# Kernel optimization log

Hardware: AMD Instinct MI355X
Metric: run time of the kernel (lower is better)

## Reference

```python
import jax, jax.numpy as jnp
import numpy as np
import math

B, L, D = 4, 512, 768
H, DH, R = 12, 64, 128


def _layernorm(x, g, b, eps=1e-5):
    mu = jnp.mean(x, axis=-1, keepdims=True)
    var = jnp.var(x, axis=-1, keepdims=True)
    return (x - mu) * jax.lax.rsqrt(var + eps) * g + b


def setup_inputs() -> dict:
    key = jax.random.key(0)
    ks = jax.random.split(key, 8)
    s = 0.02
    return {
        "x": jax.random.normal(ks[0], (B, L, D), jnp.float32),
        "W_qkv": jax.random.normal(ks[1], (D, 3 * D), jnp.float32) * s,
        "b_qkv": jnp.zeros((3 * D,), jnp.float32),
        "W_b1": jax.random.normal(ks[2], (D, R), jnp.float32) * s,
        "W_b2": jax.random.normal(ks[3], (R, H * 5), jnp.float32) * s,
        "temperature": jnp.ones((1,), jnp.float32) * 0.5,
        "W_proj": jax.random.normal(ks[4], (D, D), jnp.float32) * s,
        "b_proj": jnp.zeros((D,), jnp.float32),
        "ln_g": jnp.ones((D,), jnp.float32),
        "ln_b": jnp.zeros((D,), jnp.float32),
        "mem_g": jnp.ones((DH,), jnp.float32),
        "mem_b": jnp.zeros((DH,), jnp.float32),
    }


def reference(x, W_qkv, b_qkv, W_b1, W_b2, temperature, W_proj, b_proj, ln_g, ln_b, mem_g, mem_b):
    Bq, Lq, Dq = x.shape
    xn = _layernorm(x, ln_g, ln_b)
    qkv = xn @ W_qkv + b_qkv
    q, k, v = jnp.split(qkv, 3, axis=-1)

    # bottleneck gating params: (B, L, H, 5)
    params = (jax.nn.silu(x @ W_b1) @ W_b2).reshape(Bq, Lq, H, 5)
    sem_amp = jax.nn.sigmoid(params[..., 0])
    sem_phase = jnp.tanh(params[..., 1]) * math.pi
    ctx_amp = jax.nn.sigmoid(params[..., 2])
    ctx_phase = jnp.tanh(params[..., 3]) * math.pi
    decay = 0.5 + 0.49 * jax.nn.sigmoid(params[..., 4])  # (B,L,H)

    temp = jnp.clip(temperature, 0.1, 2.0)  # (1,) broadcasts
    interference = jnp.tanh(sem_amp * ctx_amp * jnp.cos(sem_phase - ctx_phase)) * temp
    gate = jax.nn.sigmoid(interference)  # (B,L,H)

    qf = (jax.nn.elu(q) + 1.0).reshape(Bq, Lq, H, DH)
    kf = (jax.nn.elu(k) + 1.0).reshape(Bq, Lq, H, DH)
    vf = v.reshape(Bq, Lq, H, DH)

    log_decay = jnp.log(decay + 1e-8)
    cld = jnp.maximum(jnp.cumsum(log_decay, axis=1), -85.0)  # (B,L,H)
    df = jnp.exp(cld)
    inv_df = jnp.exp(-cld)
    ema = 1.0 - decay  # (B,L,H)

    # kv outer products gated by interference: (B,L,H,DH,DH)
    kv_all = jnp.einsum('blhd,blhe->blhde', kf, vf) * (1.0 + gate)[..., None, None]
    kv_states = jnp.cumsum(kv_all * (ema * inv_df)[..., None, None], axis=1) * df[..., None, None]

    z_states = jnp.cumsum(kf * (ema * inv_df)[..., None], axis=1) * df[..., None]  # (B,L,H,DH)

    out_num = jnp.einsum('blhd,blhde->blhe', qf, kv_states)
    den = jnp.sum(qf * z_states, axis=-1, keepdims=True) + 1e-6
    out = out_num / den  # (B,L,H,DH)

    out = _layernorm(out, mem_g, mem_b)
    attn_out = out.reshape(Bq, Lq, Dq)
    return attn_out @ W_proj + b_proj, gate
```

## Files before the change

### kernel.cpp

```cpp
#include <hip/hip_runtime.h>
#include <math.h>

#define PI_F 3.14159265358979323846f

static constexpr int L_ = 512, D_ = 768, H_ = 12, DH_ = 64;
static constexpr int BL_ = 2048;
static constexpr int BLD_ = BL_ * D_;
static constexpr int NC_ = 8;
static constexpr int BH_ = 48;

__global__ void sentinel_kernel(float* out, float code, float aux) {
  out[0] = code; out[1] = aux;
}

__global__ __launch_bounds__(256) void ln_stats(const float* __restrict__ x,
                                                float* __restrict__ murs) {
  int row = blockIdx.x, tid = threadIdx.x;
  const float* xr = x + (size_t)row * D_;
  float v0 = xr[tid], v1 = xr[tid + 256], v2 = xr[tid + 512];
  float s = v0 + v1 + v2;
  float s2 = v0 * v0 + v1 * v1 + v2 * v2;
#pragma unroll
  for (int off = 32; off > 0; off >>= 1) { s += __shfl_xor(s, off); s2 += __shfl_xor(s2, off); }
  __shared__ float red[8];
  if ((tid & 63) == 0) { red[tid >> 6] = s; red[4 + (tid >> 6)] = s2; }
  __syncthreads();
  if (tid == 0) {
    float st = red[0] + red[1] + red[2] + red[3];
    float qt = red[4] + red[5] + red[6] + red[7];
    float mu = st * (1.0f / D_);
    float var = qt * (1.0f / D_) - mu * mu;
    murs[2 * row] = mu;
    murs[2 * row + 1] = rsqrtf(var + 1e-5f);
  }
}

__global__ __launch_bounds__(128) void gemm_qkv(const float* __restrict__ x,
                                                const float* __restrict__ murs,
                                                const float* __restrict__ lg,
                                                const float* __restrict__ lb,
                                                const float* __restrict__ Bm,
                                                const float* __restrict__ bias,
                                                float* __restrict__ Oq,
                                                float* __restrict__ Ok,
                                                float* __restrict__ Ov) {
  const int N = 2304, K = 768;
  __shared__ float As[16][68];
  __shared__ float Bs[16][68];
  int tid = threadIdx.x;
  int tx = tid & 15, ty = tid >> 4;
  int row0 = blockIdx.y * 64, col0 = blockIdx.x * 64;
  float acc[8][4] = {};
  int ar = tid >> 1, ak = (tid & 1) * 8;
  int bk = tid >> 3, bc = (tid & 7) * 8;
  float2 m2 = *(const float2*)&murs[2 * (row0 + ar)];
  float mu = m2.x, rs = m2.y;
  const float* Arow = x + (size_t)(row0 + ar) * K;
  for (int k0 = 0; k0 < K; k0 += 16) {
    float4 a0 = *(const float4*)&Arow[k0 + ak];
    float4 a1 = *(const float4*)&Arow[k0 + ak + 4];
    float4 g0 = *(const float4*)&lg[k0 + ak];
    float4 g1 = *(const float4*)&lg[k0 + ak + 4];
    float4 c0 = *(const float4*)&lb[k0 + ak];
    float4 c1 = *(const float4*)&lb[k0 + ak + 4];
    a0.x = (a0.x - mu) * rs * g0.x + c0.x;
    a0.y = (a0.y - mu) * rs * g0.y + c0.y;
    a0.z = (a0.z - mu) * rs * g0.z + c0.z;
    a0.w = (a0.w - mu) * rs * g0.w + c0.w;
    a1.x = (a1.x - mu) * rs * g1.x + c1.x;
    a1.y = (a1.y - mu) * rs * g1.y + c1.y;
    a1.z = (a1.z - mu) * rs * g1.z + c1.z;
    a1.w = (a1.w - mu) * rs * g1.w + c1.w;
    As[ak + 0][ar] = a0.x; As[ak + 1][ar] = a0.y;
    As[ak + 2][ar] = a0.z; As[ak + 3][ar] = a0.w;
    As[ak + 4][ar] = a1.x; As[ak + 5][ar] = a1.y;
    As[ak + 6][ar] = a1.z; As[ak + 7][ar] = a1.w;
    *(float4*)&Bs[bk][bc]     = *(const float4*)&Bm[(size_t)(k0 + bk) * N + col0 + bc];
    *(float4*)&Bs[bk][bc + 4] = *(const float4*)&Bm[(size_t)(k0 + bk) * N + col0 + bc + 4];
    __syncthreads();
#pragma unroll
    for (int kk = 0; kk < 16; ++kk) {
      float4 av0 = *(float4*)&As[kk][ty * 8];
      float4 av1 = *(float4*)&As[kk][ty * 8 + 4];
      float4 bv = *(float4*)&Bs[kk][tx * 4];
      acc[0][0] += av0.x * bv.x; acc[0][1] += av0.x * bv.y; acc[0][2] += av0.x * bv.z; acc[0][3] += av0.x * bv.w;
      acc[1][0] += av0.y * bv.x; acc[1][1] += av0.y * bv.y; acc[1][2] += av0.y * bv.z; acc[1][3] += av0.y * bv.w;
      acc[2][0] += av0.z * bv.x; acc[2][1] += av0.z * bv.y; acc[2][2] += av0.z * bv.z; acc[2][3] += av0.z * bv.w;
      acc[3][0] += av0.w * bv.x; acc[3][1] += av0.w * bv.y; acc[3][2] += av0.w * bv.z; acc[3][3] += av0.w * bv.w;
      acc[4][0] += av1.x * bv.x; acc[4][1] += av1.x * bv.y; acc[4][2] += av1.x * bv.z; acc[4][3] += av1.x * bv.w;
      acc[5][0] += av1.y * bv.x; acc[5][1] += av1.y * bv.y; acc[5][2] += av1.y * bv.z; acc[5][3] += av1.y * bv.w;
      acc[6][0] += av1.z * bv.x; acc[6][1] += av1.z * bv.y; acc[6][2] += av1.z * bv.z; acc[6][3] += av1.z * bv.w;
      acc[7][0] += av1.w * bv.x; acc[7][1] += av1.w * bv.y; acc[7][2] += av1.w * bv.z; acc[7][3] += av1.w * bv.w;
    }
    __syncthreads();
  }
  int sec = col0 / 768;
  float* O = (sec == 0) ? Oq : ((sec == 1) ? Ok : Ov);
  int lc = col0 - sec * 768 + tx * 4;
  float4 bi = *(const float4*)&bias[col0 + tx * 4];
#pragma unroll
  for (int i = 0; i < 8; ++i) {
    int r = row0 + ty * 8 + i;
    float4 v;
    v.x = acc[i][0] + bi.x; v.y = acc[i][1] + bi.y;
    v.z = acc[i][2] + bi.z; v.w = acc[i][3] + bi.w;
    if (sec < 2) {
      v.x = (v.x > 0.f) ? v.x + 1.f : expf(v.x);
      v.y = (v.y > 0.f) ? v.y + 1.f : expf(v.y);
      v.z = (v.z > 0.f) ? v.z + 1.f : expf(v.z);
      v.w = (v.w > 0.f) ? v.w + 1.f : expf(v.w);
    }
    *(float4*)&O[(size_t)r * 768 + lc] = v;
  }
}

template <int MODE>
__global__ __launch_bounds__(256) void gemm_fast(const float* __restrict__ A,
                                                 const float* __restrict__ Bm,
                                                 const float* __restrict__ bias,
                                                 float* __restrict__ O0,
                                                 int N, int K) {
  __shared__ float As[16][68];
  __shared__ float Bs[16][68];
  int tid = threadIdx.x;
  int tx = tid & 15, ty = tid >> 4;
  int row0 = blockIdx.y * 64, col0 = blockIdx.x * 64;
  float acc[4][4] = {};
  int ar = tid >> 2, ak = (tid & 3) * 4;
  int bk = tid >> 4, bc = (tid & 15) * 4;
  for (int k0 = 0; k0 < K; k0 += 16) {
    float4 a4 = *(const float4*)&A[(size_t)(row0 + ar) * K + k0 + ak];
    As[ak + 0][ar] = a4.x; As[ak + 1][ar] = a4.y;
    As[ak + 2][ar] = a4.z; As[ak + 3][ar] = a4.w;
    *(float4*)&Bs[bk][bc] = *(const float4*)&Bm[(size_t)(k0 + bk) * N + col0 + bc];
    __syncthreads();
#pragma unroll
    for (int kk = 0; kk < 16; ++kk) {
      float4 av = *(float4*)&As[kk][ty * 4];
      float4 bv = *(float4*)&Bs[kk][tx * 4];
      acc[0][0] += av.x * bv.x; acc[0][1] += av.x * bv.y; acc[0][2] += av.x * bv.z; acc[0][3] += av.x * bv.w;
      acc[1][0] += av.y * bv.x; acc[1][1] += av.y * bv.y; acc[1][2] += av.y * bv.z; acc[1][3] += av.y * bv.w;
      acc[2][0] += av.z * bv.x; acc[2][1] += av.z * bv.y; acc[2][2] += av.z * bv.z; acc[2][3] += av.z * bv.w;
      acc[3][0] += av.w * bv.x; acc[3][1] += av.w * bv.y; acc[3][2] += av.w * bv.z; acc[3][3] += av.w * bv.w;
    }
    __syncthreads();
  }
  if (MODE == 1) {
#pragma unroll
    for (int ii = 0; ii < 4; ++ii) {
      int r = row0 + ty * 4 + ii;
      float4 v;
      v.x = acc[ii][0]; v.y = acc[ii][1]; v.z = acc[ii][2]; v.w = acc[ii][3];
      v.x = v.x / (1.f + expf(-v.x));
      v.y = v.y / (1.f + expf(-v.y));
      v.z = v.z / (1.f + expf(-v.z));
      v.w = v.w / (1.f + expf(-v.w));
      *(float4*)&O0[(size_t)r * N + col0 + tx * 4] = v;
    }
  } else {
    float b0 = bias[col0 + tx * 4 + 0], b1 = bias[col0 + tx * 4 + 1];
    float b2 = bias[col0 + tx * 4 + 2], b3 = bias[col0 + tx * 4 + 3];
#pragma unroll
    for (int ii = 0; ii < 4; ++ii) {
      int r = row0 + ty * 4 + ii;
      float4 v;
      v.x = acc[ii][0] + b0; v.y = acc[ii][1] + b1;
      v.z = acc[ii][2] + b2; v.w = acc[ii][3] + b3;
      *(float4*)&O0[(size_t)r * N + col0 + tx * 4] = v;
    }
  }
}

__global__ __launch_bounds__(64) void params_kernel(const float* __restrict__ h1,
                                                    const float* __restrict__ Wb2,
                                                    const float* __restrict__ temp_p,
                                                    float* __restrict__ gate_out,
                                                    float* __restrict__ cg,
                                                    float* __restrict__ ce,
                                                    float* __restrict__ ld) {
  int t = blockIdx.x;
  int tid = threadIdx.x;
  __shared__ float hs[128];
  __shared__ float ps[60];
  *(float2*)&hs[tid * 2] = *(const float2*)&h1[(size_t)t * 128 + tid * 2];
  __syncthreads();
  if (tid < 60) {
    float acc = 0.f;
#pragma unroll 4
    for (int k = 0; k < 128; ++k) acc += hs[k] * Wb2[k * 60 + tid];
    ps[tid] = acc;
  }
  __syncthreads();
  if (tid < 12) {
    float p0 = ps[tid * 5 + 0], p1 = ps[tid * 5 + 1], p2 = ps[tid * 5 + 2];
    float p3 = ps[tid * 5 + 3], p4 = ps[tid * 5 + 4];
    float sa = 1.f / (1.f + expf(-p0));
    float sp = tanhf(p1) * PI_F;
    float ca = 1.f / (1.f + expf(-p2));
    float cp = tanhf(p3) * PI_F;
    float dec = 0.5f + 0.49f / (1.f + expf(-p4));
    float tmp = fminf(fmaxf(temp_p[0], 0.1f), 2.0f);
    float inter = tanhf(sa * ca * cosf(sp - cp)) * tmp;
    float gate = 1.f / (1.f + expf(-inter));
    gate_out[t * 12 + tid] = gate;
    int b = t >> 9, l = t & 511;
    int bhl = (b * 12 + tid) * L_ + l;
    float ema = 1.f - dec;
    cg[bhl] = ema * (1.f + gate);
    ce[bhl] = ema;
    ld[bhl] = logf(dec + 1e-8f);
  }
}

__global__ __launch_bounds__(64) void cld_kernel(const float* __restrict__ ld,
                                                 float* __restrict__ cld,
                                                 float* __restrict__ cEnd) {
  int bh = blockIdx.x;
  int lane = threadIdx.x;
  const float* src = ld + (size_t)bh * L_;
  float v[8];
  float s = 0.f;
#pragma unroll
  for (int i = 0; i < 8; ++i) { v[i] = src[lane * 8 + i]; s += v[i]; }
  float tot = s;
#pragma unroll
  for (int off = 1; off < 64; off <<= 1) {
    float n = __shfl_up(tot, off);
    if (lane >= off) tot += n;
  }
  float run = tot - s;
  float out7 = 0.f;
#pragma unroll
  for (int i = 0; i < 8; ++i) {
    run += v[i];
    float o = fmaxf(run, -85.f);
    cld[(size_t)bh * L_ + lane * 8 + i] = o;
    out7 = o;
  }
  if ((lane & 7) == 7) cEnd[bh * NC_ + (lane >> 3)] = out7;
}

__global__ __launch_bounds__(64) void infscan_kernel(const float* __restrict__ kf,
                                                     const float* __restrict__ ce,
                                                     const float* __restrict__ cld,
                                                     int* __restrict__ tstar) {
  int bh = blockIdx.x;
  int b = bh / H_, h = bh - b * H_;
  int e = threadIdx.x;
  float cz = 0.f;
  int tf = L_;
  for (int t = 0; t < L_; ++t) {
    int idx = bh * L_ + t;
    float s = ce[idx] * expf(-cld[idx]);
    float kv = kf[(size_t)(b * L_ + t) * D_ + h * DH_ + e];
    cz = cz + kv * s;
    if (tf == L_ && isinf(cz)) tf = t;
  }
#pragma unroll
  for (int off = 1; off < 64; off <<= 1) tf = min(tf, __shfl_xor(tf, off));
  if (e == 0) tstar[bh] = tf;
}

__global__ __launch_bounds__(256) void chunk_sum_kernel(const float* __restrict__ kf,
                                                        const float* __restrict__ vf,
                                                        const float* __restrict__ cg,
                                                        const float* __restrict__ ce,
                                                        const float* __restrict__ cld,
                                                        const float* __restrict__ cEnd,
                                                        float* __restrict__ T,
                                                        float* __restrict__ zc) {
  int blk = blockIdx.x;
  int c = blk & 7, bh = blk >> 3;
  int b = bh / H_, h = bh - b * H_;
  int tid = threadIdx.x;
  __shared__ float kfs[64][68];
  __shared__ float vfs[64][68];
  __shared__ float wv[64], wz[64];
  float cend = cEnd[blk];
  if (tid < 64) {
    int idx = bh * L_ + c * 64 + tid;
    float w = expf(cend - cld[idx]);
    wv[tid] = cg[idx] * w;
    wz[tid] = ce[idx] * w;
  }
  __syncthreads();
  int t = tid >> 2, g4 = (tid & 3) * 16;
  size_t rowb = (size_t)(b * L_ + c * 64 + t) * D_ + h * 64 + g4;
  float wvt = wv[t];
#pragma unroll
  for (int i = 0; i < 4; ++i) {
    *(float4*)&kfs[t][g4 + 4 * i] = *(const float4*)&kf[rowb + 4 * i];
    float4 vv = *(const float4*)&vf[rowb + 4 * i];
    vv.x *= wvt; vv.y *= wvt; vv.z *= wvt; vv.w *= wvt;
    *(float4*)&vfs[t][g4 + 4 * i] = vv;
  }
  __syncthreads();
  int d = tid >> 2, eb = (tid & 3) * 16;
  float4 a0 = {}, a1 = {}, a2 = {}, a3 = {};
  for (int tt = 0; tt < 64; ++tt) {
    float kd = kfs[tt][d];
    float4 x0 = *(float4*)&vfs[tt][eb + 0];
    float4 x1 = *(float4*)&vfs[tt][eb + 4];
    float4 x2 = *(float4*)&vfs[tt][eb + 8];
    float4 x3 = *(float4*)&vfs[tt][eb + 12];
    a0.x += kd * x0.x; a0.y += kd * x0.y; a0.z += kd * x0.z; a0.w += kd * x0.w;
    a1.x += kd * x1.x; a1.y += kd * x1.y; a1.z += kd * x1.z; a1.w += kd * x1.w;
    a2.x += kd * x2.x; a2.y += kd * x2.y; a2.z += kd * x2.z; a2.w += kd * x2.w;
    a3.x += kd * x3.x; a3.y += kd * x3.y; a3.z += kd * x3.z; a3.w += kd * x3.w;
  }
  size_t tb = (size_t)blk * 4096 + (size_t)d * 64 + eb;
  *(float4*)&T[tb + 0] = a0;
  *(float4*)&T[tb + 4] = a1;
  *(float4*)&T[tb + 8] = a2;
  *(float4*)&T[tb + 12] = a3;
  if (tid < 64) {
    float za = 0.f;
#pragma unroll 8
    for (int tt = 0; tt < 64; ++tt) za += kfs[tt][tid] * wz[tt];
    zc[blk * 64 + tid] = za;
  }
}

__global__ __launch_bounds__(256) void scan_kernel(float* __restrict__ T,
                                                   const float* __restrict__ zc,
                                                   const float* __restrict__ cEnd,
                                                   float* __restrict__ zprev) {
  int bh = blockIdx.x, tid = threadIdx.x;
  float4 s0 = {}, s1 = {}, s2 = {}, s3 = {};
  float zs = 0.f;
  float prevEnd = 0.f;
  for (int c = 0; c < NC_; ++c) {
    int blk = bh * NC_ + c;
    float r = expf(cEnd[blk] - prevEnd);
    prevEnd = cEnd[blk];
    size_t base = (size_t)blk * 4096 + (size_t)tid * 16;
    float4 t0 = *(const float4*)&T[base + 0];
    float4 t1 = *(const float4*)&T[base + 4];
    float4 t2 = *(const float4*)&T[base + 8];
    float4 t3 = *(const float4*)&T[base + 12];
    *(float4*)&T[base + 0] = s0;
    *(float4*)&T[base + 4] = s1;
    *(float4*)&T[base + 8] = s2;
    *(float4*)&T[base + 12] = s3;
    s0.x = s0.x * r + t0.x; s0.y = s0.y * r + t0.y; s0.z = s0.z * r + t0.z; s0.w = s0.w * r + t0.w;
    s1.x = s1.x * r + t1.x; s1.y = s1.y * r + t1.y; s1.z = s1.z * r + t1.z; s1.w = s1.w * r + t1.w;
    s2.x = s2.x * r + t2.x; s2.y = s2.y * r + t2.y; s2.z = s2.z * r + t2.z; s2.w = s2.w * r + t2.w;
    s3.x = s3.x * r + t3.x; s3.y = s3.y * r + t3.y; s3.z = s3.z * r + t3.z; s3.w = s3.w * r + t3.w;
    if (tid < 64) {
      zprev[blk * 64 + tid] = zs;
      zs = zs * r + zc[blk * 64 + tid];
    }
  }
}

__global__ __launch_bounds__(256) void chunk_out_kernel(const float* __restrict__ qf,
                                                        const float* __restrict__ kf,
                                                        const float* __restrict__ vf,
                                                        const float* __restrict__ cg,
                                                        const float* __restrict__ ce,
                                                        const float* __restrict__ cld,
                                                        const float* __restrict__ cEnd,
                                                        const float* __restrict__ Sprev,
                                                        const float* __restrict__ zprev,
                                                        const int* __restrict__ tstar,
                                                        const float* __restrict__ mg,
                                                        const float* __restrict__ mb,
                                                        float* __restrict__ attn) {
  int blk = blockIdx.x;
  int c = blk & 7, bh = blk >> 3;
  int b = bh / H_, h = bh - b * H_;
  int tid = threadIdx.x;
  __shared__ float qfs[64][68];
  __shared__ float kfs[64][68];
  __shared__ float vfs[64][68];
  __shared__ float cldS[64], cgS[64], ceS[64], zS[64];
  int t = tid >> 2, g4 = (tid & 3) * 16;
  size_t rowb = (size_t)(b * L_ + c * 64 + t) * D_ + h * 64 + g4;
#pragma unroll
  for (int i = 0; i < 4; ++i) {
    *(float4*)&qfs[t][g4 + 4 * i] = *(const float4*)&qf[rowb + 4 * i];
    *(float4*)&kfs[t][g4 + 4 * i] = *(const float4*)&kf[rowb + 4 * i];
    *(float4*)&vfs[t][g4 + 4 * i] = *(const float4*)&vf[rowb + 4 * i];
  }
  if (tid < 64) {
    int idx = bh * L_ + c * 64 + tid;
    cldS[tid] = cld[idx];
    cgS[tid] = cg[idx];
    ceS[tid] = ce[idx];
    zS[tid] = zprev[blk * 64 + tid];
  }
  __syncthreads();
  float prevEnd = (c == 0) ? 0.f : cEnd[blk - 1];
  int ts = tstar[bh];
  int i = tid >> 2, jb = (tid & 3) * 16;
  float sc[16];
#pragma unroll
  for (int jj = 0; jj < 16; ++jj) sc[jj] = 0.f;
  for (int d = 0; d < 64; d += 4) {
    float4 q4 = *(float4*)&qfs[i][d];
#pragma unroll
    for (int jj = 0; jj < 16; ++jj) {
      float4 k4 = *(float4*)&kfs[jb + jj][d];
      sc[jj] += q4.x * k4.x + q4.y * k4.y + q4.z * k4.z + q4.w * k4.w;
    }
  }
  float cldi = cldS[i];
  float den = 0.f;
  float mvals[16];
#pragma unroll
  for (int jj = 0; jj < 16; ++jj) {
    int j = jb + jj;
    float w = (j <= i) ? expf(cldi - cldS[j]) : 0.f;
    float sw = sc[jj] * w;
    den += sw * ceS[j];
    mvals[jj] = sw * cgS[j];
  }
  float dz = 0.f;
#pragma unroll
  for (int dd = 0; dd < 16; ++dd) dz += qfs[i][jb + dd] * zS[jb + dd];
  den += __shfl_xor(den, 1); den += __shfl_xor(den, 2);
  dz += __shfl_xor(dz, 1);  dz += __shfl_xor(dz, 2);
  float wi = expf(cldi - prevEnd);
  den += wi * dz + 1e-6f;
  __syncthreads();
#pragma unroll
  for (int jj = 0; jj < 16; ++jj) kfs[i][jb + jj] = mvals[jj];
  __syncthreads();
  float4 o0 = {}, o1 = {}, o2 = {}, o3 = {};
  for (int j = 0; j < 64; ++j) {
    float m = kfs[i][j];
    float4 x0 = *(float4*)&vfs[j][jb + 0];
    float4 x1 = *(float4*)&vfs[j][jb + 4];
    float4 x2 = *(float4*)&vfs[j][jb + 8];
    float4 x3 = *(float4*)&vfs[j][jb + 12];
    o0.x += m * x0.x; o0.y += m * x0.y; o0.z += m * x0.z; o0.w += m * x0.w;
    o1.x += m * x1.x; o1.y += m * x1.y; o1.z += m * x1.z; o1.w += m * x1.w;
    o2.x += m * x2.x; o2.y += m * x2.y; o2.z += m * x2.z; o2.w += m * x2.w;
    o3.x += m * x3.x; o3.y += m * x3.y; o3.z += m * x3.z; o3.w += m * x3.w;
  }
  float4 p0 = {}, p1 = {}, p2 = {}, p3 = {};
  size_t sb = (size_t)blk * 4096;
  for (int d = 0; d < 64; ++d) {
    float qd = qfs[i][d];
    float4 x0 = *(const float4*)&Sprev[sb + d * 64 + jb + 0];
    float4 x1 = *(const float4*)&Sprev[sb + d * 64 + jb + 4];
    float4 x2 = *(const float4*)&Sprev[sb + d * 64 + jb + 8];
    float4 x3 = *(const float4*)&Sprev[sb + d * 64 + jb + 12];
    p0.x += qd * x0.x; p0.y += qd * x0.y; p0.z += qd * x0.z; p0.w += qd * x0.w;
    p1.x += qd * x1.x; p1.y += qd * x1.y; p1.z += qd * x1.z; p1.w += qd * x1.w;
    p2.x += qd * x2.x; p2.y += qd * x2.y; p2.z += qd * x2.z; p2.w += qd * x2.w;
    p3.x += qd * x3.x; p3.y += qd * x3.y; p3.z += qd * x3.z; p3.w += qd * x3.w;
  }
  size_t ob = (size_t)(b * L_ + c * 64 + i) * D_ + h * 64 + jb;
  if (c * 64 + i >= ts) {
#pragma unroll
    for (int q4i = 0; q4i < 4; ++q4i) {
      float4 w4;
      w4.x = mb[jb + q4i * 4 + 0]; w4.y = mb[jb + q4i * 4 + 1];
      w4.z = mb[jb + q4i * 4 + 2]; w4.w = mb[jb + q4i * 4 + 3];
      *(float4*)&attn[ob + q4i * 4] = w4;
    }
    return;
  }
  float inv = 1.0f / den;
  float o[16];
  o[0] = (o0.x + wi * p0.x) * inv;  o[1] = (o0.y + wi * p0.y) * inv;
  o[2] = (o0.z + wi * p0.z) * inv;  o[3] = (o0.w + wi * p0.w) * inv;
  o[4] = (o1.x + wi * p1.x) * inv;  o[5] = (o1.y + wi * p1.y) * inv;
  o[6] = (o1.z + wi * p1.z) * inv;  o[7] = (o1.w + wi * p1.w) * inv;
  o[8] = (o2.x + wi * p2.x) * inv;  o[9] = (o2.y + wi * p2.y) * inv;
  o[10] = (o2.z + wi * p2.z) * inv; o[11] = (o2.w + wi * p2.w) * inv;
  o[12] = (o3.x + wi * p3.x) * inv; o[13] = (o3.y + wi * p3.y) * inv;
  o[14] = (o3.z + wi * p3.z) * inv; o[15] = (o3.w + wi * p3.w) * inv;
  float s = 0.f, s2 = 0.f;
#pragma unroll
  for (int e2 = 0; e2 < 16; ++e2) { s += o[e2]; s2 += o[e2] * o[e2]; }
  s += __shfl_xor(s, 1);  s += __shfl_xor(s, 2);
  s2 += __shfl_xor(s2, 1); s2 += __shfl_xor(s2, 2);
  float mu = s * (1.f / 64.f);
  float var = s2 * (1.f / 64.f) - mu * mu;
  float rs = rsqrtf(var + 1e-5f);
#pragma unroll
  for (int q4i = 0; q4i < 4; ++q4i) {
    float4 w4;
    w4.x = (o[q4i * 4 + 0] - mu) * rs * mg[jb + q4i * 4 + 0] + mb[jb + q4i * 4 + 0];
    w4.y = (o[q4i * 4 + 1] - mu) * rs * mg[jb + q4i * 4 + 1] + mb[jb + q4i * 4 + 1];
    w4.z = (o[q4i * 4 + 2] - mu) * rs * mg[jb + q4i * 4 + 2] + mb[jb + q4i * 4 + 2];
    w4.w = (o[q4i * 4 + 3] - mu) * rs * mg[jb + q4i * 4 + 3] + mb[jb + q4i * 4 + 3];
    *(float4*)&attn[ob + q4i * 4] = w4;
  }
}

extern "C" void kernel_launch(void* const* d_in, const int* in_sizes, int n_in,
                              void* d_out, int out_size, void* d_ws, size_t ws_size,
                              hipStream_t stream) {
  const float* x     = (const float*)d_in[0];
  const float* Wqkv  = (const float*)d_in[1];
  const float* bqkv  = (const float*)d_in[2];
  const float* Wb1   = (const float*)d_in[3];
  const float* Wb2   = (const float*)d_in[4];
  const float* temp  = (const float*)d_in[5];
  const float* Wproj = (const float*)d_in[6];
  const float* bproj = (const float*)d_in[7];
  const float* lng   = (const float*)d_in[8];
  const float* lnb   = (const float*)d_in[9];
  const float* memg  = (const float*)d_in[10];
  const float* memb  = (const float*)d_in[11];
  float* out0 = (float*)d_out;
  float* gate = out0 + BLD_;

  static const int expect[12] = {1572864, 1769472, 2304, 98304, 7680, 1,
                                 589824, 768, 768, 768, 64, 64};
  int bad = (n_in == 12) ? -1 : 99;
  if (bad < 0) for (int i = 0; i < 12; ++i) if (in_sizes[i] != expect[i]) { bad = i; break; }
  size_t need = (size_t)(4 * BLD_ + 262144 + 4 * 24576) * sizeof(float);
  if (bad >= 0) { sentinel_kernel<<<1, 1, 0, stream>>>(out0, 3.0e6f, (float)bad); return; }
  if (ws_size < need) { sentinel_kernel<<<1, 1, 0, stream>>>(out0, 1.0e6f, (float)(ws_size >> 20)); return; }

  float* ws   = (float*)d_ws;
  float* xn   = ws;
  float* qfb  = xn + BLD_;
  float* kfb  = qfb + BLD_;
  float* vfb  = kfb + BLD_;
  float* h1   = vfb + BLD_;
  float* cgb  = h1 + 262144;
  float* ceb  = cgb + 24576;
  float* ldb  = ceb + 24576;
  float* cldb = ldb + 24576;
  float* murs = xn;
  float* Tb   = xn;
  float* zcb  = h1;
  float* zpv  = h1 + 24576;
  float* cEnd = h1 + 49152;
  int*   tstar = (int*)(h1 + 49536);
  float* attn = qfb;

  ln_stats<<<BL_, 256, 0, stream>>>(x, murs);
  gemm_fast<1><<<dim3(2, 32), 256, 0, stream>>>(x, Wb1, nullptr, h1, 128, 768);
  params_kernel<<<BL_, 64, 0, stream>>>(h1, Wb2, temp, gate, cgb, ceb, ldb);
  cld_kernel<<<BH_, 64, 0, stream>>>(ldb, cldb, cEnd);
  gemm_qkv<<<dim3(36, 32), 128, 0, stream>>>(x, murs, lng, lnb, Wqkv, bqkv, qfb, kfb, vfb);
  infscan_kernel<<<BH_, 64, 0, stream>>>(kfb, ceb, cldb, tstar);
  chunk_sum_kernel<<<BH_ * NC_, 256, 0, stream>>>(kfb, vfb, cgb, ceb, cldb, cEnd, Tb, zcb);
  scan_kernel<<<BH_, 256, 0, stream>>>(Tb, zcb, cEnd, zpv);
  chunk_out_kernel<<<BH_ * NC_, 256, 0, stream>>>(qfb, kfb, vfb, cgb, ceb, cldb, cEnd,
                                                  Tb, zpv, tstar, memg, memb, attn);
  gemm_fast<2><<<dim3(12, 32), 256, 0, stream>>>(attn, Wproj, bproj, out0, 768, 768);
}
```

Measured before the change: 466.9 us.

## Fuse bottleneck GEMM with params kernel and retile QKV GEMM to 256 threads

Replaces the separate x@W_b1 tiled GEMM plus params kernel with one per-token kernel that loads the row into shared memory, does the 768x128 matvec with SiLU, then the 128x60 projection and gating math. This removes one launch and the h1 round-trip through global memory, but each block now rereads all of W_b1 from cache with no tile reuse. The QKV GEMM moves from 128 threads with 8x4 micro-tiles to 256 threads with 4x4 micro-tiles. That raises thread-level parallelism but lowers register reuse per thread.

```diff
diff --git a/kernel.cpp b/kernel.cpp
--- a/kernel.cpp
+++ b/kernel.cpp
@@ -35,7 +35,57 @@
   }
 }
 
-__global__ __launch_bounds__(128) void gemm_qkv(const float* __restrict__ x,
+__global__ __launch_bounds__(128) void bottleneck_kernel(const float* __restrict__ x,
+                                                         const float* __restrict__ Wb1,
+                                                         const float* __restrict__ Wb2,
+                                                         const float* __restrict__ temp_p,
+                                                         float* __restrict__ gate_out,
+                                                         float* __restrict__ cg,
+                                                         float* __restrict__ ce,
+                                                         float* __restrict__ ld) {
+  int t = blockIdx.x;
+  int tid = threadIdx.x;
+  __shared__ float xs[768];
+  __shared__ float hs[128];
+  __shared__ float ps[60];
+  const float* xr = x + (size_t)t * D_;
+#pragma unroll
+  for (int i = 0; i < 6; ++i) xs[tid + i * 128] = xr[tid + i * 128];
+  __syncthreads();
+  float acc = 0.f;
+#pragma unroll 8
+  for (int k = 0; k < 768; ++k) acc += xs[k] * Wb1[k * 128 + tid];
+  hs[tid] = acc / (1.f + expf(-acc));
+  __syncthreads();
+  if (tid < 60) {
+    float a = 0.f;
+#pragma unroll 4
+    for (int k = 0; k < 128; ++k) a += hs[k] * Wb2[k * 60 + tid];
+    ps[tid] = a;
+  }
+  __syncthreads();
+  if (tid < 12) {
+    float p0 = ps[tid * 5 + 0], p1 = ps[tid * 5 + 1], p2 = ps[tid * 5 + 2];
+    float p3 = ps[tid * 5 + 3], p4 = ps[tid * 5 + 4];
+    float sa = 1.f / (1.f + expf(-p0));
+    float sp = tanhf(p1) * PI_F;
+    float ca = 1.f / (1.f + expf(-p2));
+    float cp = tanhf(p3) * PI_F;
+    float dec = 0.5f + 0.49f / (1.f + expf(-p4));
+    float tmp = fminf(fmaxf(temp_p[0], 0.1f), 2.0f);
+    float inter = tanhf(sa * ca * cosf(sp - cp)) * tmp;
+    float gate = 1.f / (1.f + expf(-inter));
+    gate_out[t * 12 + tid] = gate;
+    int b = t >> 9, l = t & 511;
+    int bhl = (b * 12 + tid) * L_ + l;
+    float ema = 1.f - dec;
+    cg[bhl] = ema * (1.f + gate);
+    ce[bhl] = ema;
+    ld[bhl] = logf(dec + 1e-8f);
+  }
+}
+
+__global__ __launch_bounds__(256) void gemm_qkv(const float* __restrict__ x,
                                                 const float* __restrict__ murs,
                                                 const float* __restrict__ lg,
                                                 const float* __restrict__ lb,
@@ -50,60 +100,46 @@
   int tid = threadIdx.x;
   int tx = tid & 15, ty = tid >> 4;
   int row0 = blockIdx.y * 64, col0 = blockIdx.x * 64;
-  float acc[8][4] = {};
-  int ar = tid >> 1, ak = (tid & 1) * 8;
-  int bk = tid >> 3, bc = (tid & 7) * 8;
+  float acc[4][4] = {};
+  int ar = tid >> 2, ak = (tid & 3) * 4;
+  int bk = tid >> 4, bc = (tid & 15) * 4;
   float2 m2 = *(const float2*)&murs[2 * (row0 + ar)];
   float mu = m2.x, rs = m2.y;
   const float* Arow = x + (size_t)(row0 + ar) * K;
   for (int k0 = 0; k0 < K; k0 += 16) {
-    float4 a0 = *(const float4*)&Arow[k0 + ak];
-    float4 a1 = *(const float4*)&Arow[k0 + ak + 4];
-    float4 g0 = *(const float4*)&lg[k0 + ak];
-    float4 g1 = *(const float4*)&lg[k0 + ak + 4];
-    float4 c0 = *(const float4*)&lb[k0 + ak];
-    float4 c1 = *(const float4*)&lb[k0 + ak + 4];
-    a0.x = (a0.x - mu) * rs * g0.x + c0.x;
-    a0.y = (a0.y - mu) * rs * g0.y + c0.y;
-    a0.z = (a0.z - mu) * rs * g0.z + c0.z;
-    a0.w = (a0.w - mu) * rs * g0.w + c0.w;
-    a1.x = (a1.x - mu) * rs * g1.x + c1.x;
-    a1.y = (a1.y - mu) * rs * g1.y + c1.y;
-    a1.z = (a1.z - mu) * rs * g1.z + c1.z;
-    a1.w = (a1.w - mu) * rs * g1.w + c1.w;
-    As[ak + 0][ar] = a0.x; As[ak + 1][ar] = a0.y;
-    As[ak + 2][ar] = a0.z; As[ak + 3][ar] = a0.w;
-    As[ak + 4][ar] = a1.x; As[ak + 5][ar] = a1.y;
-    As[ak + 6][ar] = a1.z; As[ak + 7][ar] = a1.w;
-    *(float4*)&Bs[bk][bc]     = *(const float4*)&Bm[(size_t)(k0 + bk) * N + col0 + bc];
-    *(float4*)&Bs[bk][bc + 4] = *(const float4*)&Bm[(size_t)(k0 + bk) * N + col0 + bc + 4];
+    float4 a4 = *(const float4*)&Arow[k0 + ak];
+    float4 g4 = *(const float4*)&lg[k0 + ak];
+    float4 c4 = *(const float4*)&lb[k0 + ak];
+    a4.x = (a4.x - mu) * rs * g4.x + c4.x;
+    a4.y = (a4.y - mu) * rs * g4.y + c4.y;
+    a4.z = (a4.z - mu) * rs * g4.z + c4.z;
+    a4.w = (a4.w - mu) * rs * g4.w + c4.w;
+    As[ak + 0][ar] = a4.x; As[ak + 1][ar] = a4.y;
+    As[ak + 2][ar] = a4.z; As[ak + 3][ar] = a4.w;
+    *(float4*)&Bs[bk][bc] = *(const float4*)&Bm[(size_t)(k0 + bk) * N + col0 + bc];
     __syncthreads();
 #pragma unroll
     for (int kk = 0; kk < 16; ++kk) {
-      float4 av0 = *(float4*)&As[kk][ty * 8];
-      float4 av1 = *(float4*)&As[kk][ty * 8 + 4];
+      float4 av = *(float4*)&As[kk][ty * 4];
       float4 bv = *(float4*)&Bs[kk][tx * 4];
-      acc[0][0] += av0.x * bv.x; acc[0][1] += av0.x * bv.y; acc[0][2] += av0.x * bv.z; acc[0][3] += av0.x * bv.w;
-      acc[1][0] += av0.y * bv.x; acc[1][1] += av0.y * bv.y; acc[1][2] += av0.y * bv.z; acc[1][3] += av0.y * bv.w;
-      acc[2][0] += av0.z * bv.x; acc[2][1] += av0.z * bv.y; acc[2][2] += av0.z * bv.z; acc[2][3] += av0.z * bv.w;
-      acc[3][0] += av0.w * bv.x; acc[3][1] += av0.w * bv.y; acc[3][2] += av0.w * bv.z; acc[3][3] += av0.w * bv.w;
-      acc[4][0] += av1.x * bv.x; acc[4][1] += av1.x * bv.y; acc[4][2] += av1.x * bv.z; acc[4][3] += av1.x * bv.w;
-      acc[5][0] += av1.y * bv.x; acc[5][1] += av1.y * bv.y; acc[5][2] += av1.y * bv.z; acc[5][3] += av1.y * bv.w;
-      acc[6][0] += av1.z * bv.x; acc[6][1] += av1.z * bv.y; acc[6][2] += av1.z * bv.z; acc[6][3] += av1.z * bv.w;
-      acc[7][0] += av1.w * bv.x; acc[7][1] += av1.w * bv.y; acc[7][2] += av1.w * bv.z; acc[7][3] += av1.w * bv.w;
+      acc[0][0] += av.x * bv.x; acc[0][1] += av.x * bv.y; acc[0][2] += av.x * bv.z; acc[0][3] += av.x * bv.w;
+      acc[1][0] += av.y * bv.x; acc[1][1] += av.y * bv.y; acc[1][2] += av.y * bv.z; acc[1][3] += av.y * bv.w;
+      acc[2][0] += av.z * bv.x; acc[2][1] += av.z * bv.y; acc[2][2] += av.z * bv.z; acc[2][3] += av.z * bv.w;
+      acc[3][0] += av.w * bv.x; acc[3][1] += av.w * bv.y; acc[3][2] += av.w * bv.z; acc[3][3] += av.w * bv.w;
     }
     __syncthreads();
   }
   int sec = col0 / 768;
   float* O = (sec == 0) ? Oq : ((sec == 1) ? Ok : Ov);
   int lc = col0 - sec * 768 + tx * 4;
-  float4 bi = *(const float4*)&bias[col0 + tx * 4];
-#pragma unroll
-  for (int i = 0; i < 8; ++i) {
-    int r = row0 + ty * 8 + i;
+  float b0 = bias[col0 + tx * 4 + 0], b1 = bias[col0 + tx * 4 + 1];
+  float b2 = bias[col0 + tx * 4 + 2], b3 = bias[col0 + tx * 4 + 3];
+#pragma unroll
+  for (int ii = 0; ii < 4; ++ii) {
+    int r = row0 + ty * 4 + ii;
     float4 v;
-    v.x = acc[i][0] + bi.x; v.y = acc[i][1] + bi.y;
-    v.z = acc[i][2] + bi.z; v.w = acc[i][3] + bi.w;
+    v.x = acc[ii][0] + b0; v.y = acc[ii][1] + b1;
+    v.z = acc[ii][2] + b2; v.w = acc[ii][3] + b3;
     if (sec < 2) {
       v.x = (v.x > 0.f) ? v.x + 1.f : expf(v.x);
       v.y = (v.y > 0.f) ? v.y + 1.f : expf(v.y);
@@ -114,8 +150,7 @@
   }
 }
 
-template <int MODE>
-__global__ __launch_bounds__(256) void gemm_fast(const float* __restrict__ A,
+__global__ __launch_bounds__(256) void gemm_proj(const float* __restrict__ A,
                                                  const float* __restrict__ Bm,
                                                  const float* __restrict__ bias,
                                                  float* __restrict__ O0,
@@ -145,70 +180,15 @@
     }
     __syncthreads();
   }
-  if (MODE == 1) {
-#pragma unroll
-    for (int ii = 0; ii < 4; ++ii) {
-      int r = row0 + ty * 4 + ii;
-      float4 v;
-      v.x = acc[ii][0]; v.y = acc[ii][1]; v.z = acc[ii][2]; v.w = acc[ii][3];
-      v.x = v.x / (1.f + expf(-v.x));
-      v.y = v.y / (1.f + expf(-v.y));
-      v.z = v.z / (1.f + expf(-v.z));
-      v.w = v.w / (1.f + expf(-v.w));
-      *(float4*)&O0[(size_t)r * N + col0 + tx * 4] = v;
-    }
-  } else {
-    float b0 = bias[col0 + tx * 4 + 0], b1 = bias[col0 + tx * 4 + 1];
-    float b2 = bias[col0 + tx * 4 + 2], b3 = bias[col0 + tx * 4 + 3];
-#pragma unroll
-    for (int ii = 0; ii < 4; ++ii) {
-      int r = row0 + ty * 4 + ii;
-      float4 v;
-      v.x = acc[ii][0] + b0; v.y = acc[ii][1] + b1;
-      v.z = acc[ii][2] + b2; v.w = acc[ii][3] + b3;
-      *(float4*)&O0[(size_t)r * N + col0 + tx * 4] = v;
-    }
-  }
-}
-
-__global__ __launch_bounds__(64) void params_kernel(const float* __restrict__ h1,
-                                                    const float* __restrict__ Wb2,
-                                                    const float* __restrict__ temp_p,
-                                                    float* __restrict__ gate_out,
-                                                    float* __restrict__ cg,
-                                                    float* __restrict__ ce,
-                                                    float* __restrict__ ld) {
-  int t = blockIdx.x;
-  int tid = threadIdx.x;
-  __shared__ float hs[128];
-  __shared__ float ps[60];
-  *(float2*)&hs[tid * 2] = *(const float2*)&h1[(size_t)t * 128 + tid * 2];
-  __syncthreads();
-  if (tid < 60) {
-    float acc = 0.f;
-#pragma unroll 4
-    for (int k = 0; k < 128; ++k) acc += hs[k] * Wb2[k * 60 + tid];
-    ps[tid] = acc;
-  }
-  __syncthreads();
-  if (tid < 12) {
-    float p0 = ps[tid * 5 + 0], p1 = ps[tid * 5 + 1], p2 = ps[tid * 5 + 2];
-    float p3 = ps[tid * 5 + 3], p4 = ps[tid * 5 + 4];
-    float sa = 1.f / (1.f + expf(-p0));
-    float sp = tanhf(p1) * PI_F;
-    float ca = 1.f / (1.f + expf(-p2));
-    float cp = tanhf(p3) * PI_F;
-    float dec = 0.5f + 0.49f / (1.f + expf(-p4));
-    float tmp = fminf(fmaxf(temp_p[0], 0.1f), 2.0f);
-    float inter = tanhf(sa * ca * cosf(sp - cp)) * tmp;
-    float gate = 1.f / (1.f + expf(-inter));
-    gate_out[t * 12 + tid] = gate;
-    int b = t >> 9, l = t & 511;
-    int bhl = (b * 12 + tid) * L_ + l;
-    float ema = 1.f - dec;
-    cg[bhl] = ema * (1.f + gate);
-    ce[bhl] = ema;
-    ld[bhl] = logf(dec + 1e-8f);
+  float b0 = bias[col0 + tx * 4 + 0], b1 = bias[col0 + tx * 4 + 1];
+  float b2 = bias[col0 + tx * 4 + 2], b3 = bias[col0 + tx * 4 + 3];
+#pragma unroll
+  for (int ii = 0; ii < 4; ++ii) {
+    int r = row0 + ty * 4 + ii;
+    float4 v;
+    v.x = acc[ii][0] + b0; v.y = acc[ii][1] + b1;
+    v.z = acc[ii][2] + b2; v.w = acc[ii][3] + b3;
+    *(float4*)&O0[(size_t)r * N + col0 + tx * 4] = v;
   }
 }
 
@@ -536,14 +516,13 @@
   float* attn = qfb;
 
   ln_stats<<<BL_, 256, 0, stream>>>(x, murs);
-  gemm_fast<1><<<dim3(2, 32), 256, 0, stream>>>(x, Wb1, nullptr, h1, 128, 768);
-  params_kernel<<<BL_, 64, 0, stream>>>(h1, Wb2, temp, gate, cgb, ceb, ldb);
+  bottleneck_kernel<<<BL_, 128, 0, stream>>>(x, Wb1, Wb2, temp, gate, cgb, ceb, ldb);
   cld_kernel<<<BH_, 64, 0, stream>>>(ldb, cldb, cEnd);
-  gemm_qkv<<<dim3(36, 32), 128, 0, stream>>>(x, murs, lng, lnb, Wqkv, bqkv, qfb, kfb, vfb);
+  gemm_qkv<<<dim3(36, 32), 256, 0, stream>>>(x, murs, lng, lnb, Wqkv, bqkv, qfb, kfb, vfb);
   infscan_kernel<<<BH_, 64, 0, stream>>>(kfb, ceb, cldb, tstar);
   chunk_sum_kernel<<<BH_ * NC_, 256, 0, stream>>>(kfb, vfb, cgb, ceb, cldb, cEnd, Tb, zcb);
   scan_kernel<<<BH_, 256, 0, stream>>>(Tb, zcb, cEnd, zpv);
   chunk_out_kernel<<<BH_ * NC_, 256, 0, stream>>>(qfb, kfb, vfb, cgb, ceb, cldb, cEnd,
                                                   Tb, zpv, tstar, memg, memb, attn);
-  gemm_fast<2><<<dim3(12, 32), 256, 0, stream>>>(attn, Wproj, bproj, out0, 768, 768);
-}
+  gemm_proj<<<dim3(12, 32), 256, 0, stream>>>(attn, Wproj, bproj, out0, 768, 768);
+}
```

Result: faster. 416.4 us (-10.8%).
